# Kernel optimization log

Measured on AMD Instinct MI355X. Metric: run time of the kernel, lower is better.

## Reference

```python
import jax, jax.numpy as jnp
import numpy as np

GAMMA = 2.0
ALPHA = 0.25
SIZE_AVERAGE = True


def setup_inputs() -> dict:
    key = jax.random.key(0)
    k1, k2 = jax.random.split(key)
    B, C = 32768, 2048
    # probabilities strictly inside (0, 1) so log terms stay finite
    result = jax.random.uniform(k1, (B, C), dtype=jnp.float32,
                                minval=1e-4, maxval=1.0 - 1e-4)
    classes = jax.random.randint(k2, (B,), 0, C, dtype=jnp.int64)
    return {"result": result, "classes": classes}


def reference(result, classes):
    # nan -> 1e-6 (matches the in-place isnan patching in the original)
    p = jnp.where(jnp.isnan(result), jnp.float32(1e-6), result)  # [B, C]
    B, C = p.shape
    is_target = jax.nn.one_hot(classes, C, dtype=jnp.bool_)       # [B, C]
    # target class:     -alpha     * (1-p)^gamma * log(p)
    # non-target class: -(1-alpha) *  p^gamma    * log(1-p)
    pos = -ALPHA * jnp.power(1.0 - p, GAMMA) * jnp.log(p)
    neg = -(1.0 - ALPHA) * jnp.power(p, GAMMA) * jnp.log(1.0 - p)
    loss = jnp.sum(jnp.where(is_target, pos, neg))
    if SIZE_AVERAGE:
        loss = loss / B
    return loss
```

## Files before the change

kernel.cpp:

```cpp
#include <hip/hip_runtime.h>
#include <hip/hip_bf16.h>

static constexpr int BLOCK     = 256;
static constexpr int GRID_MAIN = 2048;

typedef float f32x4 __attribute__((ext_vector_type(4)));

__device__ __forceinline__ float patch_nan(float x) {
    return (x != x) ? 1e-6f : x;
}

__device__ __forceinline__ float neg_term(float x) {
    return -0.75f * x * x * __logf(1.0f - x);
}

__device__ __forceinline__ float pos_term(float x) {
    float om = 1.0f - x;
    return -0.25f * om * om * __logf(x);
}

__device__ __forceinline__ float block_reduce_sum(float v) {
    #pragma unroll
    for (int off = 32; off > 0; off >>= 1)
        v += __shfl_down(v, off, 64);
    __shared__ float smem[BLOCK / 64];
    const int lane = threadIdx.x & 63;
    const int wid  = threadIdx.x >> 6;
    if (lane == 0) smem[wid] = v;
    __syncthreads();
    float r = 0.0f;
    if (threadIdx.x == 0) {
        #pragma unroll
        for (int i = 0; i < BLOCK / 64; ++i) r += smem[i];
    }
    return r;
}

__global__ void __launch_bounds__(BLOCK)
focal_fused(const f32x4* __restrict__ p4, const int* __restrict__ classes,
            float* __restrict__ partials, int n4, int shiftC4) {
    float acc = 0.0f;
    const int maskC4  = (1 << shiftC4) - 1;
    const int stride  = gridDim.x * blockDim.x;
    for (int i = blockIdx.x * blockDim.x + threadIdx.x; i < n4; i += stride) {
        f32x4 v = __builtin_nontemporal_load(&p4[i]);
        float x0 = patch_nan(v.x), x1 = patch_nan(v.y);
        float x2 = patch_nan(v.z), x3 = patch_nan(v.w);
        acc += neg_term(x0);
        acc += neg_term(x1);
        acc += neg_term(x2);
        acc += neg_term(x3);
        const int row     = i >> shiftC4;
        const int colbase = (i & maskC4) << 2;
        const unsigned d  = (unsigned)(classes[row] - colbase);
        if (d < 4u) {
            float x = (d == 0) ? x0 : (d == 1) ? x1 : (d == 2) ? x2 : x3;
            acc += pos_term(x) - neg_term(x);
        }
    }
    float r = block_reduce_sum(acc);
    if (threadIdx.x == 0) partials[blockIdx.x] = r;
}

__global__ void __launch_bounds__(BLOCK)
focal_final(const float* __restrict__ partials, int n,
            float* __restrict__ out, float invB) {
    float acc = 0.0f;
    for (int i = threadIdx.x; i < n; i += blockDim.x) acc += partials[i];
    float r = block_reduce_sum(acc);
    if (threadIdx.x == 0) out[0] = r * invB;
}

extern "C" void kernel_launch(void* const* d_in, const int* in_sizes, int n_in,
                              void* d_out, int out_size, void* d_ws, size_t ws_size,
                              hipStream_t stream) {
    const float* p       = (const float*)d_in[0];
    const int*   classes = (const int*)d_in[1];
    float*       out     = (float*)d_out;
    float*       ws      = (float*)d_ws;

    const long long N = (long long)in_sizes[0];
    const int B  = in_sizes[1];
    const int C  = (int)(N / B);
    const int n4 = (int)(N / 4);
    const int c4 = C / 4;

    int shiftC4 = 0;
    while ((1 << shiftC4) < c4) ++shiftC4;

    focal_fused<<<GRID_MAIN, BLOCK, 0, stream>>>((const f32x4*)p, classes,
                                                 ws, n4, shiftC4);
    focal_final<<<1, BLOCK, 0, stream>>>(ws, GRID_MAIN, out, 1.0f / (float)B);
}
```

Baseline: 53.04 us.

## Add row-blocked reduction kernel with shared-memory class cache for C=2048

Adds a specialized kernel where each block handles a contiguous range of whole rows. Each thread loads two float4 per row, and the row's class indices are cached in shared memory, which removes per-element row/column index math and repeated class loads. Nontemporal loads are also dropped in favour of plain loads. The generic kernel stays as a fallback, and the new path only runs when C equals 2048 and B divides evenly by the grid.

```diff
diff --git a/kernel.cpp b/kernel.cpp
--- a/kernel.cpp
+++ b/kernel.cpp
@@ -3,6 +3,7 @@
 
 static constexpr int BLOCK     = 256;
 static constexpr int GRID_MAIN = 2048;
+static constexpr int MAX_RPB   = 32;
 
 typedef float f32x4 __attribute__((ext_vector_type(4)));
 
@@ -37,19 +38,50 @@
 }
 
 __global__ void __launch_bounds__(BLOCK)
+focal_rows(const f32x4* __restrict__ p4, const int* __restrict__ classes,
+           float* __restrict__ partials, int c4, int rpb) {
+    __shared__ int s_cls[MAX_RPB];
+    const int row0 = blockIdx.x * rpb;
+    if (threadIdx.x < rpb) s_cls[threadIdx.x] = classes[row0 + threadIdx.x];
+    __syncthreads();
+
+    const int tid = threadIdx.x;
+    const f32x4* rp = p4 + (size_t)row0 * c4 + 2 * tid;
+    float acc = 0.0f;
+
+    for (int r = 0; r < rpb; ++r, rp += c4) {
+        f32x4 v0 = rp[0];
+        f32x4 v1 = rp[1];
+        float x0 = patch_nan(v0.x), x1 = patch_nan(v0.y);
+        float x2 = patch_nan(v0.z), x3 = patch_nan(v0.w);
+        float x4 = patch_nan(v1.x), x5 = patch_nan(v1.y);
+        float x6 = patch_nan(v1.z), x7 = patch_nan(v1.w);
+        acc += neg_term(x0) + neg_term(x1) + neg_term(x2) + neg_term(x3);
+        acc += neg_term(x4) + neg_term(x5) + neg_term(x6) + neg_term(x7);
+        const unsigned d = (unsigned)(s_cls[r] - (tid << 3));
+        if (d < 8u) {
+            float x = (d == 0) ? x0 : (d == 1) ? x1 : (d == 2) ? x2 :
+                      (d == 3) ? x3 : (d == 4) ? x4 : (d == 5) ? x5 :
+                      (d == 6) ? x6 : x7;
+            acc += pos_term(x) - neg_term(x);
+        }
+    }
+
+    float r = block_reduce_sum(acc);
+    if (threadIdx.x == 0) partials[blockIdx.x] = r;
+}
+
+__global__ void __launch_bounds__(BLOCK)
 focal_fused(const f32x4* __restrict__ p4, const int* __restrict__ classes,
             float* __restrict__ partials, int n4, int shiftC4) {
     float acc = 0.0f;
-    const int maskC4  = (1 << shiftC4) - 1;
-    const int stride  = gridDim.x * blockDim.x;
-    for (int i = blockIdx.x * blockDim.x + threadIdx.x; i < n4; i += stride) {
-        f32x4 v = __builtin_nontemporal_load(&p4[i]);
+    const int maskC4 = (1 << shiftC4) - 1;
+    const int S      = gridDim.x * blockDim.x;
+    for (int i = blockIdx.x * blockDim.x + threadIdx.x; i < n4; i += S) {
+        f32x4 v = p4[i];
         float x0 = patch_nan(v.x), x1 = patch_nan(v.y);
         float x2 = patch_nan(v.z), x3 = patch_nan(v.w);
-        acc += neg_term(x0);
-        acc += neg_term(x1);
-        acc += neg_term(x2);
-        acc += neg_term(x3);
+        acc += neg_term(x0) + neg_term(x1) + neg_term(x2) + neg_term(x3);
         const int row     = i >> shiftC4;
         const int colbase = (i & maskC4) << 2;
         const unsigned d  = (unsigned)(classes[row] - colbase);
@@ -85,10 +117,18 @@
     const int n4 = (int)(N / 4);
     const int c4 = C / 4;
 
-    int shiftC4 = 0;
-    while ((1 << shiftC4) < c4) ++shiftC4;
+    const int rpb = B / GRID_MAIN;
+    const bool specialized = (c4 == 2 * BLOCK) && (B % GRID_MAIN == 0) &&
+                             (rpb <= MAX_RPB);
 
-    focal_fused<<<GRID_MAIN, BLOCK, 0, stream>>>((const f32x4*)p, classes,
-                                                 ws, n4, shiftC4);
+    if (specialized) {
+        focal_rows<<<GRID_MAIN, BLOCK, 0, stream>>>((const f32x4*)p, classes,
+                                                    ws, c4, rpb);
+    } else {
+        int shiftC4 = 0;
+        while ((1 << shiftC4) < c4) ++shiftC4;
+        focal_fused<<<GRID_MAIN, BLOCK, 0, stream>>>((const f32x4*)p, classes,
+                                                     ws, n4, shiftC4);
+    }
     focal_final<<<1, BLOCK, 0, stream>>>(ws, GRID_MAIN, out, 1.0f / (float)B);
 }
```

Measured after the change: 50.57 us, median of 2. -4.7%, faster.
